# Performance work log

Measured on AMD Instinct MI355X. Metric: run time of the kernel, lower is better.

## Reference

```python
import jax, jax.numpy as jnp
import numpy as np

B, D, R = 4096, 1024, 256
DT = 0.01
DT_SCALE = 1.0

# Yoshida 4th-order coefficients
_W1 = 1.0 / (2.0 - 2.0 ** (1.0 / 3.0))
_W0 = -(2.0 ** (1.0 / 3.0)) / (2.0 - 2.0 ** (1.0 / 3.0))
C1 = _W1 / 2.0
C2 = (_W0 + _W1) / 2.0
C3 = C2
C4 = C1
D1 = _W1
D2 = _W0
D3 = _W1


def setup_inputs() -> dict:
    key = jax.random.key(0)
    k1, k2, k3, k4, k5 = jax.random.split(key, 5)
    x = jax.random.normal(k1, (B, D), dtype=jnp.float32)
    v = jax.random.normal(k2, (B, D), dtype=jnp.float32)
    force = jax.random.normal(k3, (B, D), dtype=jnp.float32)
    # low-rank christoffel factors, scaled for numerical stability
    U = jax.random.normal(k4, (R, D), dtype=jnp.float32) * (1.0 / np.sqrt(D))
    W = jax.random.normal(k5, (D, R), dtype=jnp.float32) * (1.0 / np.sqrt(R))
    return {"x": x, "v": v, "force": force, "U": U, "W": W}


def _christoffel(tv, tx, U, W):
    # Gamma(v) = W @ (U v)^2  (low-rank quadratic form; x unused, matching
    # the gfn yoshida_fused(U, W) signature)
    h = jnp.einsum("rd,bd->br", U, tv)  # [B, R]
    return jnp.einsum("dr,br->bd", W, h * h)  # [B, D]


def reference(x, v, force, U, W):
    dt = DT * DT_SCALE

    def acceleration(tx, tv):
        return -_christoffel(tv, tx, U, W) + force

    x1 = x + C1 * dt * v
    v1 = v + D1 * dt * acceleration(x1, v)
    x2 = x1 + C2 * dt * v1
    v2 = v1 + D2 * dt * acceleration(x2, v1)
    x3 = x2 + C3 * dt * v2
    v3 = v2 + D3 * dt * acceleration(x3, v2)
    x_final = x3 + C4 * dt * v3
    return (x_final, v3)
```

## Files before the change

kernel.cpp:

```cpp
#include <hip/hip_runtime.h>


#define BSZ 4096
#define DD 1024
#define RR 256

#define U_OFF 0u
#define W_OFF (512u * 1024u)
#define M_OFF (1024u * 1024u)

typedef unsigned char uchar;
typedef long long i64;
typedef unsigned int uint;
typedef __attribute__((ext_vector_type(4))) float f32x4;
typedef __attribute__((ext_vector_type(4))) uint uint4v;
typedef __attribute__((ext_vector_type(8))) short short8;

__device__ inline uint f2bf1(float x) {
    uint u = __builtin_bit_cast(uint, x);
    return (u + 0x7FFFu + ((u >> 16) & 1u)) >> 16;
}
__device__ inline uint f2bf2(float lo, float hi) {
    return f2bf1(lo) | (f2bf1(hi) << 16);
}

__global__ __launch_bounds__(256) void pack_kernel(
    const float* __restrict__ U, const float* __restrict__ W,
    uchar* __restrict__ ws)
{
    const int g = blockIdx.x * 256 + threadIdx.x;
    *reinterpret_cast<float*>(ws + M_OFF + (size_t)g * 4) = 0.0f;

    const int l = g & 63;
    const float* src;
    size_t dst;
    if (g < 32768) {
        const int slice = g >> 6, nt = slice >> 5, p = slice & 31;
        src = U + (size_t)(nt * 16 + (l & 15)) * DD + p * 32 + (l >> 4) * 8;
        dst = U_OFF + (size_t)slice * 1024 + l * 16;
    } else {
        const int g2 = g - 32768;
        const int slice = g2 >> 6, dt_ = slice >> 3, p = slice & 7;
        src = W + (size_t)(dt_ * 16 + (l & 15)) * RR + p * 32 + (l >> 4) * 8;
        dst = W_OFF + (size_t)slice * 1024 + l * 16;
    }
    const float4 a0 = *reinterpret_cast<const float4*>(src);
    const float4 a1 = *reinterpret_cast<const float4*>(src + 4);
    uint4v o;
    o.x = f2bf2(a0.x, a0.y); o.y = f2bf2(a0.z, a0.w);
    o.z = f2bf2(a1.x, a1.y); o.w = f2bf2(a1.z, a1.w);
    *reinterpret_cast<uint4v*>(ws + dst) = o;
}

__global__ __launch_bounds__(1024) void mm_kernel(
    const float* __restrict__ U, const float* __restrict__ W,
    uchar* __restrict__ ws)
{
    float* Mf = reinterpret_cast<float*>(ws + M_OFF);
    const int rt = blockIdx.x >> 4;
    const int kc = blockIdx.x & 15;
    const int rp = threadIdx.x & 255;
    const int ro = threadIdx.x >> 8;
    float acc[4] = {0.f, 0.f, 0.f, 0.f};
    const int kb = kc * 64;
    for (int ks = 0; ks < 8; ++ks) {
        float uv[4][8];
        #pragma unroll
        for (int j = 0; j < 4; ++j) {
            const float* us = U + (size_t)(rt * 16 + ro * 4 + j) * DD + kb + ks * 8;
            const float4 u0 = *reinterpret_cast<const float4*>(us);
            const float4 u1 = *reinterpret_cast<const float4*>(us + 4);
            uv[j][0] = u0.x; uv[j][1] = u0.y; uv[j][2] = u0.z; uv[j][3] = u0.w;
            uv[j][4] = u1.x; uv[j][5] = u1.y; uv[j][6] = u1.z; uv[j][7] = u1.w;
        }
        #pragma unroll
        for (int kk = 0; kk < 8; ++kk) {
            const float wv = W[(size_t)(kb + ks * 8 + kk) * RR + rp];
            #pragma unroll
            for (int j = 0; j < 4; ++j) acc[j] += uv[j][kk] * wv;
        }
    }
    #pragma unroll
    for (int j = 0; j < 4; ++j)
        atomicAdd(Mf + (size_t)(rt * 16 + ro * 4 + j) * RR + rp, acc[j]);
}

__global__ __launch_bounds__(1024) void yoshida_fused_kernel(
    const float* __restrict__ x_in,
    const float* __restrict__ v_in,
    const float* __restrict__ force,
    const uchar* __restrict__ ws,
    float* __restrict__ x_out,
    float* __restrict__ v_out)
{
    __shared__ __align__(16) uchar lds[152 * 1024];
    uchar* const vA  = lds;
    uchar* const fA  = lds + 32768;
    uchar* const Ml  = lds;
    uchar* const H2B = lds + 131072;
    uchar* const PB  = lds + 139264;
    uchar* const QB  = lds + 147456;

    const int tid = threadIdx.x;
    const int w = tid >> 6, l = tid & 63;
    const int m = l & 15, q = l >> 4;
    const int b0 = blockIdx.x * 16;

    constexpr double CBRT2 = 1.2599210498948731647672106072782;
    constexpr double W1c = 1.0 / (2.0 - CBRT2);
    constexpr double W0c = -CBRT2 * W1c;
    constexpr double DTd = 0.01;
    constexpr double D1 = W1c, D2 = W0c, D3 = W1c;
    constexpr double C2c = (W0c + W1c) * 0.5, C4c = W1c * 0.5;
    constexpr double E1 = (C2c + C2c + C4c) * D1;
    constexpr double E2 = (C2c + C4c) * D2;
    constexpr double E3 = C4c * D3;
    const float dtf = (float)DTd, dt2 = (float)(DTd * DTd);
    const float se = (float)(E1 + E2 + E3);

    #pragma unroll
    for (int j = 0; j < 2; ++j) {
        const int p = 2 * w + j;
        const size_t so = (size_t)(b0 + m) * DD + p * 32 + q * 8;
        const float4 v0_ = *reinterpret_cast<const float4*>(v_in + so);
        const float4 v1_ = *reinterpret_cast<const float4*>(v_in + so + 4);
        const float4 f0_ = *reinterpret_cast<const float4*>(force + so);
        const float4 f1_ = *reinterpret_cast<const float4*>(force + so + 4);
        uint4v ov, of;
        ov.x = f2bf2(v0_.x, v0_.y); ov.y = f2bf2(v0_.z, v0_.w);
        ov.z = f2bf2(v1_.x, v1_.y); ov.w = f2bf2(v1_.z, v1_.w);
        of.x = f2bf2(f0_.x, f0_.y); of.y = f2bf2(f0_.z, f0_.w);
        of.z = f2bf2(f1_.x, f1_.y); of.w = f2bf2(f1_.z, f1_.w);
        *reinterpret_cast<uint4v*>(vA + (size_t)p * 1024 + l * 16) = ov;
        *reinterpret_cast<uint4v*>(fA + (size_t)p * 1024 + l * 16) = of;
    }

    const uchar* const up = ws + U_OFF + ((size_t)w << 15) + l * 16;
    uint4v ub[8];
    #pragma unroll
    for (int p = 0; p < 8; ++p)
        ub[p] = *reinterpret_cast<const uint4v*>(up + ((size_t)p << 10));

    __syncthreads();

    f32x4 h = {0.f, 0.f, 0.f, 0.f}, g = {0.f, 0.f, 0.f, 0.f};
    #pragma unroll
    for (int p = 0; p < 32; ++p) {
        const uint4v uc = ub[p & 7];
        if (p < 24)
            ub[p & 7] = *reinterpret_cast<const uint4v*>(up + ((size_t)(p + 8) << 10));
        const short8 ua = __builtin_bit_cast(short8, uc);
        const short8 va = __builtin_bit_cast(short8,
            *reinterpret_cast<const uint4v*>(vA + ((size_t)p << 10) + l * 16));
        const short8 fa = __builtin_bit_cast(short8,
            *reinterpret_cast<const uint4v*>(fA + ((size_t)p << 10) + l * 16));
        h = __builtin_amdgcn_mfma_f32_16x16x32_bf16(ua, va, h, 0, 0, 0);
        g = __builtin_amdgcn_mfma_f32_16x16x32_bf16(ua, fa, g, 0, 0, 0);
    }

    __syncthreads();

    {
        const float* Mf = reinterpret_cast<const float*>(ws + M_OFF);
        #pragma unroll 4
        for (int rep = 0; rep < 8; ++rep) {
            const int item = tid + rep * 1024;
            const int sl = item >> 6, ll = item & 63;
            const int nt = sl >> 3, p = sl & 7;
            const float* sm = Mf + (size_t)(nt * 16 + (ll & 15)) * RR + p * 32 + (ll >> 4) * 8;
            const float4 a0 = *reinterpret_cast<const float4*>(sm);
            const float4 a1 = *reinterpret_cast<const float4*>(sm + 4);
            uint4v o;
            o.x = f2bf2(a0.x, a0.y); o.y = f2bf2(a0.z, a0.w);
            o.z = f2bf2(a1.x, a1.y); o.w = f2bf2(a1.z, a1.w);
            *reinterpret_cast<uint4v*>(Ml + (size_t)sl * 1024 + ll * 16) = o;
        }
    }

    const int k0 = 16 * w + 4 * q;
    const int p0 = k0 >> 5;
    const int lp = ((k0 & 31) >> 3) * 16 + m;
    const int j0 = k0 & 7;

    f32x4 P, Q;
    {
        float h2[4];
        #pragma unroll
        for (int i = 0; i < 4; ++i) h2[i] = h[i] * h[i];
        #pragma unroll
        for (int i = 0; i < 4; ++i) {
            P[i] = (float)D1 * h2[i];
            Q[i] = (float)E1 * h2[i];
        }
        *reinterpret_cast<uint*>(H2B + (size_t)p0 * 1024 + lp * 16 + j0 * 2)
            = f2bf2(h2[0], h2[1]);
        *reinterpret_cast<uint*>(H2B + (size_t)p0 * 1024 + lp * 16 + j0 * 2 + 4)
            = f2bf2(h2[2], h2[3]);
    }
    __syncthreads();
    {
        f32x4 acc = {0.f, 0.f, 0.f, 0.f};
        #pragma unroll
        for (int p = 0; p < 8; ++p) {
            const short8 ma = __builtin_bit_cast(short8,
                *reinterpret_cast<const uint4v*>(Ml + (size_t)(w * 8 + p) * 1024 + l * 16));
            const short8 hb = __builtin_bit_cast(short8,
                *reinterpret_cast<const uint4v*>(H2B + ((size_t)p << 10) + l * 16));
            acc = __builtin_amdgcn_mfma_f32_16x16x32_bf16(ma, hb, acc, 0, 0, 0);
        }
        const float cg = (float)(DTd * D1);
        #pragma unroll
        for (int i = 0; i < 4; ++i) h[i] += cg * (g[i] - acc[i]);
    }
    __syncthreads();
    {
        float h2[4];
        #pragma unroll
        for (int i = 0; i < 4; ++i) h2[i] = h[i] * h[i];
        #pragma unroll
        for (int i = 0; i < 4; ++i) {
            P[i] += (float)D2 * h2[i];
            Q[i] += (float)E2 * h2[i];
        }
        *reinterpret_cast<uint*>(H2B + (size_t)p0 * 1024 + lp * 16 + j0 * 2)
            = f2bf2(h2[0], h2[1]);
        *reinterpret_cast<uint*>(H2B + (size_t)p0 * 1024 + lp * 16 + j0 * 2 + 4)
            = f2bf2(h2[2], h2[3]);
    }
    __syncthreads();
    {
        f32x4 acc = {0.f, 0.f, 0.f, 0.f};
        #pragma unroll
        for (int p = 0; p < 8; ++p) {
            const short8 ma = __builtin_bit_cast(short8,
                *reinterpret_cast<const uint4v*>(Ml + (size_t)(w * 8 + p) * 1024 + l * 16));
            const short8 hb = __builtin_bit_cast(short8,
                *reinterpret_cast<const uint4v*>(H2B + ((size_t)p << 10) + l * 16));
            acc = __builtin_amdgcn_mfma_f32_16x16x32_bf16(ma, hb, acc, 0, 0, 0);
        }
        const float cg = (float)(DTd * D2);
        #pragma unroll
        for (int i = 0; i < 4; ++i) h[i] += cg * (g[i] - acc[i]);
    }
    {
        float h2[4];
        #pragma unroll
        for (int i = 0; i < 4; ++i) h2[i] = h[i] * h[i];
        #pragma unroll
        for (int i = 0; i < 4; ++i) {
            P[i] += (float)D3 * h2[i];
            Q[i] += (float)E3 * h2[i];
        }
    }
    *reinterpret_cast<uint*>(PB + (size_t)p0 * 1024 + lp * 16 + j0 * 2)     = f2bf2(P[0], P[1]);
    *reinterpret_cast<uint*>(PB + (size_t)p0 * 1024 + lp * 16 + j0 * 2 + 4) = f2bf2(P[2], P[3]);
    *reinterpret_cast<uint*>(QB + (size_t)p0 * 1024 + lp * 16 + j0 * 2)     = f2bf2(Q[0], Q[1]);
    *reinterpret_cast<uint*>(QB + (size_t)p0 * 1024 + lp * 16 + j0 * 2 + 4) = f2bf2(Q[2], Q[3]);

    const uchar* const wpb = ws + W_OFF + l * 16;
    uint4v wb[4][2];
    #pragma unroll
    for (int p = 0; p < 4; ++p) {
        wb[p][0] = *reinterpret_cast<const uint4v*>(wpb + (size_t)((4 * w)     * 8 + p) * 1024);
        wb[p][1] = *reinterpret_cast<const uint4v*>(wpb + (size_t)((4 * w + 1) * 8 + p) * 1024);
    }

    __syncthreads();

    #pragma unroll
    for (int half = 0; half < 2; ++half) {
        const int t0 = 4 * w + half * 2;
        f32x4 aV[2] = {{0.f,0.f,0.f,0.f}, {0.f,0.f,0.f,0.f}};
        f32x4 aX[2] = {{0.f,0.f,0.f,0.f}, {0.f,0.f,0.f,0.f}};
        #pragma unroll
        for (int p = 0; p < 8; ++p) {
            const uint4v c0 = wb[p & 3][0];
            const uint4v c1 = wb[p & 3][1];
            if (p < 4) {
                wb[p & 3][0] = *reinterpret_cast<const uint4v*>(
                    wpb + (size_t)((t0)     * 8 + p + 4) * 1024);
                wb[p & 3][1] = *reinterpret_cast<const uint4v*>(
                    wpb + (size_t)((t0 + 1) * 8 + p + 4) * 1024);
            } else if (half == 0) {
                wb[p & 3][0] = *reinterpret_cast<const uint4v*>(
                    wpb + (size_t)((t0 + 2) * 8 + (p - 4)) * 1024);
                wb[p & 3][1] = *reinterpret_cast<const uint4v*>(
                    wpb + (size_t)((t0 + 3) * 8 + (p - 4)) * 1024);
            }
            const short8 pb = __builtin_bit_cast(short8,
                *reinterpret_cast<const uint4v*>(PB + ((size_t)p << 10) + l * 16));
            const short8 qb = __builtin_bit_cast(short8,
                *reinterpret_cast<const uint4v*>(QB + ((size_t)p << 10) + l * 16));
            const short8 w0 = __builtin_bit_cast(short8, c0);
            const short8 w1 = __builtin_bit_cast(short8, c1);
            aV[0] = __builtin_amdgcn_mfma_f32_16x16x32_bf16(w0, pb, aV[0], 0, 0, 0);
            aV[1] = __builtin_amdgcn_mfma_f32_16x16x32_bf16(w1, pb, aV[1], 0, 0, 0);
            aX[0] = __builtin_amdgcn_mfma_f32_16x16x32_bf16(w0, qb, aX[0], 0, 0, 0);
            aX[1] = __builtin_amdgcn_mfma_f32_16x16x32_bf16(w1, qb, aX[1], 0, 0, 0);
        }
        #pragma unroll
        for (int t = 0; t < 2; ++t) {
            const int d0 = (t0 + t) * 16 + 4 * q;
            #pragma unroll
            for (int i = 0; i < 4; ++i) {
                const size_t gi = (size_t)(b0 + m) * DD + d0 + i;
                const float fv = force[gi];
                const float v0 = v_in[gi];
                const float x0 = x_in[gi];
                v_out[gi] = v0 + dtf * fv - dtf * aV[t][i];
                x_out[gi] = x0 + dtf * v0 + dt2 * se * fv - dt2 * aX[t][i];
            }
        }
    }
}

extern "C" void kernel_launch(void* const* d_in, const int* in_sizes, int n_in,
                              void* d_out, int out_size, void* d_ws, size_t ws_size,
                              hipStream_t stream) {
    const float* x     = (const float*)d_in[0];
    const float* v     = (const float*)d_in[1];
    const float* force = (const float*)d_in[2];
    const float* U     = (const float*)d_in[3];
    const float* W     = (const float*)d_in[4];

    float* x_out = (float*)d_out;
    float* v_out = x_out + (size_t)BSZ * DD;

    uchar* ws = (uchar*)d_ws;

    pack_kernel<<<dim3(256), dim3(256), 0, stream>>>(U, W, ws);
    mm_kernel<<<dim3(256), dim3(1024), 0, stream>>>(U, W, ws);
    yoshida_fused_kernel<<<dim3(BSZ / 16), dim3(1024), 0, stream>>>(
        x, v, force, ws, x_out, v_out);
}
```

Measured before the change: 148.5 us.

## Shrink LDS footprint, stream v/force from global, precompute packed bf16 M

The M = U·W product is now computed by a non-atomic kernel that writes bf16 directly in MFMA fragment layout, so the zero-init and the in-kernel fp32-to-bf16 repack of M are gone. The main kernel no longer stages v and force in LDS. It converts them on the fly from global loads and keeps M fragments in registers, cutting LDS from 152KB to 24KB, which allows more blocks per CU. Output writes are vectorized to float4. The risks are higher register pressure, a slower uncoalesced single-output-per-thread matmul, and strided global loads inside the MFMA loop.

Result: slower. 242.8 us (+63.5%).

```diff
diff --git a/kernel.cpp b/kernel.cpp
--- a/kernel.cpp
+++ b/kernel.cpp
@@ -10,8 +10,8 @@
 #define M_OFF (1024u * 1024u)
 
 typedef unsigned char uchar;
-typedef long long i64;
 typedef unsigned int uint;
+typedef unsigned short ushort;
 typedef __attribute__((ext_vector_type(4))) float f32x4;
 typedef __attribute__((ext_vector_type(4))) uint uint4v;
 typedef __attribute__((ext_vector_type(8))) short short8;
@@ -22,6 +22,17 @@
 }
 __device__ inline uint f2bf2(float lo, float hi) {
     return f2bf1(lo) | (f2bf1(hi) << 16);
+}
+__device__ inline uint cvt2(float a, float b) {
+    const __bf16 lo = (__bf16)a, hi = (__bf16)b;
+    return (uint)__builtin_bit_cast(ushort, lo) |
+           ((uint)__builtin_bit_cast(ushort, hi) << 16);
+}
+__device__ inline uint4v frag8(const float4 a, const float4 b) {
+    uint4v o;
+    o.x = cvt2(a.x, a.y); o.y = cvt2(a.z, a.w);
+    o.z = cvt2(b.x, b.y); o.w = cvt2(b.z, b.w);
+    return o;
 }
 
 __global__ __launch_bounds__(256) void pack_kernel(
@@ -29,8 +40,6 @@
     uchar* __restrict__ ws)
 {
     const int g = blockIdx.x * 256 + threadIdx.x;
-    *reinterpret_cast<float*>(ws + M_OFF + (size_t)g * 4) = 0.0f;
-
     const int l = g & 63;
     const float* src;
     size_t dst;
@@ -56,33 +65,27 @@
     const float* __restrict__ U, const float* __restrict__ W,
     uchar* __restrict__ ws)
 {
-    float* Mf = reinterpret_cast<float*>(ws + M_OFF);
-    const int rt = blockIdx.x >> 4;
-    const int kc = blockIdx.x & 15;
-    const int rp = threadIdx.x & 255;
-    const int ro = threadIdx.x >> 8;
-    float acc[4] = {0.f, 0.f, 0.f, 0.f};
-    const int kb = kc * 64;
-    for (int ks = 0; ks < 8; ++ks) {
-        float uv[4][8];
-        #pragma unroll
-        for (int j = 0; j < 4; ++j) {
-            const float* us = U + (size_t)(rt * 16 + ro * 4 + j) * DD + kb + ks * 8;
-            const float4 u0 = *reinterpret_cast<const float4*>(us);
-            const float4 u1 = *reinterpret_cast<const float4*>(us + 4);
-            uv[j][0] = u0.x; uv[j][1] = u0.y; uv[j][2] = u0.z; uv[j][3] = u0.w;
-            uv[j][4] = u1.x; uv[j][5] = u1.y; uv[j][6] = u1.z; uv[j][7] = u1.w;
-        }
-        #pragma unroll
-        for (int kk = 0; kk < 8; ++kk) {
-            const float wv = W[(size_t)(kb + ks * 8 + kk) * RR + rp];
-            #pragma unroll
-            for (int j = 0; j < 4; ++j) acc[j] += uv[j][kk] * wv;
-        }
-    }
-    #pragma unroll
-    for (int j = 0; j < 4; ++j)
-        atomicAdd(Mf + (size_t)(rt * 16 + ro * 4 + j) * RR + rp, acc[j]);
+    const int rt = blockIdx.x >> 2;
+    const int cc = blockIdx.x & 3;
+    const int r  = rt * 16 + (threadIdx.x >> 6);
+    const int c  = cc * 64 + (threadIdx.x & 63);
+    const float* ur = U + (size_t)r * DD;
+    const float* wc = W + c;
+    float acc = 0.f;
+    #pragma unroll 2
+    for (int k = 0; k < DD; k += 8) {
+        const float4 u0 = *reinterpret_cast<const float4*>(ur + k);
+        const float4 u1 = *reinterpret_cast<const float4*>(ur + k + 4);
+        float wv[8];
+        #pragma unroll
+        for (int j = 0; j < 8; ++j) wv[j] = wc[(size_t)(k + j) * RR];
+        acc += u0.x * wv[0] + u0.y * wv[1] + u0.z * wv[2] + u0.w * wv[3]
+             + u1.x * wv[4] + u1.y * wv[5] + u1.z * wv[6] + u1.w * wv[7];
+    }
+    const int slice = ((r >> 4) << 3) + (c >> 5);
+    const int ll = (r & 15) | (((c >> 3) & 3) << 4);
+    *reinterpret_cast<ushort*>(ws + M_OFF + (size_t)slice * 1024 + ll * 16 + (c & 7) * 2)
+        = (ushort)f2bf1(acc);
 }
 
 __global__ __launch_bounds__(1024) void yoshida_fused_kernel(
@@ -93,13 +96,9 @@
     float* __restrict__ x_out,
     float* __restrict__ v_out)
 {
-    __shared__ __align__(16) uchar lds[152 * 1024];
-    uchar* const vA  = lds;
-    uchar* const fA  = lds + 32768;
-    uchar* const Ml  = lds;
-    uchar* const H2B = lds + 131072;
-    uchar* const PB  = lds + 139264;
-    uchar* const QB  = lds + 147456;
+    __shared__ __align__(16) uchar H2B[8192];
+    __shared__ __align__(16) uchar PB[8192];
+    __shared__ __align__(16) uchar QB[8192];
 
     const int tid = threadIdx.x;
     const int w = tid >> 6, l = tid & 63;
@@ -118,69 +117,37 @@
     const float dtf = (float)DTd, dt2 = (float)(DTd * DTd);
     const float se = (float)(E1 + E2 + E3);
 
-    #pragma unroll
-    for (int j = 0; j < 2; ++j) {
-        const int p = 2 * w + j;
-        const size_t so = (size_t)(b0 + m) * DD + p * 32 + q * 8;
-        const float4 v0_ = *reinterpret_cast<const float4*>(v_in + so);
-        const float4 v1_ = *reinterpret_cast<const float4*>(v_in + so + 4);
-        const float4 f0_ = *reinterpret_cast<const float4*>(force + so);
-        const float4 f1_ = *reinterpret_cast<const float4*>(force + so + 4);
-        uint4v ov, of;
-        ov.x = f2bf2(v0_.x, v0_.y); ov.y = f2bf2(v0_.z, v0_.w);
-        ov.z = f2bf2(v1_.x, v1_.y); ov.w = f2bf2(v1_.z, v1_.w);
-        of.x = f2bf2(f0_.x, f0_.y); of.y = f2bf2(f0_.z, f0_.w);
-        of.z = f2bf2(f1_.x, f1_.y); of.w = f2bf2(f1_.z, f1_.w);
-        *reinterpret_cast<uint4v*>(vA + (size_t)p * 1024 + l * 16) = ov;
-        *reinterpret_cast<uint4v*>(fA + (size_t)p * 1024 + l * 16) = of;
-    }
-
-    const uchar* const up = ws + U_OFF + ((size_t)w << 15) + l * 16;
-    uint4v ub[8];
-    #pragma unroll
-    for (int p = 0; p < 8; ++p)
+    const float* vsrc = v_in  + (size_t)(b0 + m) * DD + q * 8;
+    const float* fsrc = force + (size_t)(b0 + m) * DD + q * 8;
+    const uchar* const up = ws + U_OFF + ((size_t)(w * 32) << 10) + l * 16;
+
+    uint4v ub[4];
+    #pragma unroll
+    for (int p = 0; p < 4; ++p)
         ub[p] = *reinterpret_cast<const uint4v*>(up + ((size_t)p << 10));
 
-    __syncthreads();
-
     f32x4 h = {0.f, 0.f, 0.f, 0.f}, g = {0.f, 0.f, 0.f, 0.f};
     #pragma unroll
     for (int p = 0; p < 32; ++p) {
-        const uint4v uc = ub[p & 7];
-        if (p < 24)
-            ub[p & 7] = *reinterpret_cast<const uint4v*>(up + ((size_t)(p + 8) << 10));
+        const uint4v uc = ub[p & 3];
+        if (p < 28)
+            ub[p & 3] = *reinterpret_cast<const uint4v*>(up + ((size_t)(p + 4) << 10));
+        const float4 v0 = *reinterpret_cast<const float4*>(vsrc + p * 32);
+        const float4 v1 = *reinterpret_cast<const float4*>(vsrc + p * 32 + 4);
+        const float4 f0 = *reinterpret_cast<const float4*>(fsrc + p * 32);
+        const float4 f1 = *reinterpret_cast<const float4*>(fsrc + p * 32 + 4);
         const short8 ua = __builtin_bit_cast(short8, uc);
-        const short8 va = __builtin_bit_cast(short8,
-            *reinterpret_cast<const uint4v*>(vA + ((size_t)p << 10) + l * 16));
-        const short8 fa = __builtin_bit_cast(short8,
-            *reinterpret_cast<const uint4v*>(fA + ((size_t)p << 10) + l * 16));
+        const short8 va = __builtin_bit_cast(short8, frag8(v0, v1));
+        const short8 fa = __builtin_bit_cast(short8, frag8(f0, f1));
         h = __builtin_amdgcn_mfma_f32_16x16x32_bf16(ua, va, h, 0, 0, 0);
         g = __builtin_amdgcn_mfma_f32_16x16x32_bf16(ua, fa, g, 0, 0, 0);
-    }
-
-    __syncthreads();
-
-    {
-        const float* Mf = reinterpret_cast<const float*>(ws + M_OFF);
-        #pragma unroll 4
-        for (int rep = 0; rep < 8; ++rep) {
-            const int item = tid + rep * 1024;
-            const int sl = item >> 6, ll = item & 63;
-            const int nt = sl >> 3, p = sl & 7;
-            const float* sm = Mf + (size_t)(nt * 16 + (ll & 15)) * RR + p * 32 + (ll >> 4) * 8;
-            const float4 a0 = *reinterpret_cast<const float4*>(sm);
-            const float4 a1 = *reinterpret_cast<const float4*>(sm + 4);
-            uint4v o;
-            o.x = f2bf2(a0.x, a0.y); o.y = f2bf2(a0.z, a0.w);
-            o.z = f2bf2(a1.x, a1.y); o.w = f2bf2(a1.z, a1.w);
-            *reinterpret_cast<uint4v*>(Ml + (size_t)sl * 1024 + ll * 16) = o;
-        }
     }
 
     const int k0 = 16 * w + 4 * q;
     const int p0 = k0 >> 5;
     const int lp = ((k0 & 31) >> 3) * 16 + m;
     const int j0 = k0 & 7;
+    uchar* const h2w0 = H2B + (size_t)p0 * 1024 + lp * 16 + j0 * 2;
 
     f32x4 P, Q;
     {
@@ -192,21 +159,25 @@
             P[i] = (float)D1 * h2[i];
             Q[i] = (float)E1 * h2[i];
         }
-        *reinterpret_cast<uint*>(H2B + (size_t)p0 * 1024 + lp * 16 + j0 * 2)
-            = f2bf2(h2[0], h2[1]);
-        *reinterpret_cast<uint*>(H2B + (size_t)p0 * 1024 + lp * 16 + j0 * 2 + 4)
-            = f2bf2(h2[2], h2[3]);
-    }
+        *reinterpret_cast<uint*>(h2w0)     = f2bf2(h2[0], h2[1]);
+        *reinterpret_cast<uint*>(h2w0 + 4) = f2bf2(h2[2], h2[3]);
+    }
+
+    const uchar* const mp = ws + M_OFF + ((size_t)(w * 8) << 10) + l * 16;
+    uint4v mb[8];
+    #pragma unroll
+    for (int p = 0; p < 8; ++p)
+        mb[p] = *reinterpret_cast<const uint4v*>(mp + ((size_t)p << 10));
+
     __syncthreads();
     {
         f32x4 acc = {0.f, 0.f, 0.f, 0.f};
         #pragma unroll
         for (int p = 0; p < 8; ++p) {
-            const short8 ma = __builtin_bit_cast(short8,
-                *reinterpret_cast<const uint4v*>(Ml + (size_t)(w * 8 + p) * 1024 + l * 16));
             const short8 hb = __builtin_bit_cast(short8,
                 *reinterpret_cast<const uint4v*>(H2B + ((size_t)p << 10) + l * 16));
-            acc = __builtin_amdgcn_mfma_f32_16x16x32_bf16(ma, hb, acc, 0, 0, 0);
+            acc = __builtin_amdgcn_mfma_f32_16x16x32_bf16(
+                      __builtin_bit_cast(short8, mb[p]), hb, acc, 0, 0, 0);
         }
         const float cg = (float)(DTd * D1);
         #pragma unroll
@@ -222,21 +193,18 @@
             P[i] += (float)D2 * h2[i];
             Q[i] += (float)E2 * h2[i];
         }
-        *reinterpret_cast<uint*>(H2B + (size_t)p0 * 1024 + lp * 16 + j0 * 2)
-            = f2bf2(h2[0], h2[1]);
-        *reinterpret_cast<uint*>(H2B + (size_t)p0 * 1024 + lp * 16 + j0 * 2 + 4)
-            = f2bf2(h2[2], h2[3]);
+        *reinterpret_cast<uint*>(h2w0)     = f2bf2(h2[0], h2[1]);
+        *reinterpret_cast<uint*>(h2w0 + 4) = f2bf2(h2[2], h2[3]);
     }
     __syncthreads();
     {
         f32x4 acc = {0.f, 0.f, 0.f, 0.f};
         #pragma unroll
         for (int p = 0; p < 8; ++p) {
-            const short8 ma = __builtin_bit_cast(short8,
-                *reinterpret_cast<const uint4v*>(Ml + (size_t)(w * 8 + p) * 1024 + l * 16));
             const short8 hb = __builtin_bit_cast(short8,
                 *reinterpret_cast<const uint4v*>(H2B + ((size_t)p << 10) + l * 16));
-            acc = __builtin_amdgcn_mfma_f32_16x16x32_bf16(ma, hb, acc, 0, 0, 0);
+            acc = __builtin_amdgcn_mfma_f32_16x16x32_bf16(
+                      __builtin_bit_cast(short8, mb[p]), hb, acc, 0, 0, 0);
         }
         const float cg = (float)(DTd * D2);
         #pragma unroll
@@ -300,16 +268,21 @@
         }
         #pragma unroll
         for (int t = 0; t < 2; ++t) {
-            const int d0 = (t0 + t) * 16 + 4 * q;
-            #pragma unroll
-            for (int i = 0; i < 4; ++i) {
-                const size_t gi = (size_t)(b0 + m) * DD + d0 + i;
-                const float fv = force[gi];
-                const float v0 = v_in[gi];
-                const float x0 = x_in[gi];
-                v_out[gi] = v0 + dtf * fv - dtf * aV[t][i];
-                x_out[gi] = x0 + dtf * v0 + dt2 * se * fv - dt2 * aX[t][i];
-            }
+            const size_t gib = (size_t)(b0 + m) * DD + (t0 + t) * 16 + 4 * q;
+            const float4 fv = *reinterpret_cast<const float4*>(force + gib);
+            const float4 v0 = *reinterpret_cast<const float4*>(v_in + gib);
+            const float4 x0 = *reinterpret_cast<const float4*>(x_in + gib);
+            float4 vo, xo;
+            vo.x = v0.x + dtf * fv.x - dtf * aV[t][0];
+            vo.y = v0.y + dtf * fv.y - dtf * aV[t][1];
+            vo.z = v0.z + dtf * fv.z - dtf * aV[t][2];
+            vo.w = v0.w + dtf * fv.w - dtf * aV[t][3];
+            xo.x = x0.x + dtf * v0.x + dt2 * se * fv.x - dt2 * aX[t][0];
+            xo.y = x0.y + dtf * v0.y + dt2 * se * fv.y - dt2 * aX[t][1];
+            xo.z = x0.z + dtf * v0.z + dt2 * se * fv.z - dt2 * aX[t][2];
+            xo.w = x0.w + dtf * v0.w + dt2 * se * fv.w - dt2 * aX[t][3];
+            *reinterpret_cast<float4*>(v_out + gib) = vo;
+            *reinterpret_cast<float4*>(x_out + gib) = xo;
         }
     }
 }
@@ -328,8 +301,8 @@
 
     uchar* ws = (uchar*)d_ws;
 
-    pack_kernel<<<dim3(256), dim3(256), 0, stream>>>(U, W, ws);
-    mm_kernel<<<dim3(256), dim3(1024), 0, stream>>>(U, W, ws);
+    pack_kernel<<<dim3(192), dim3(256), 0, stream>>>(U, W, ws);
+    mm_kernel<<<dim3(64), dim3(1024), 0, stream>>>(U, W, ws);
     yoshida_fused_kernel<<<dim3(BSZ / 16), dim3(1024), 0, stream>>>(
         x, v, force, ws, x_out, v_out);
 }
```
